# Optimization experiments

Hardware: AMD Instinct MI355X
Metric: run time of the kernel (lower is better)

## Reference

```python
import jax, jax.numpy as jnp
import numpy as np

N_CELL = 66
N_SUB = 29934
N = N_CELL + N_SUB  # 30000 nodes
F = 256
E_HALF = 480000
K = 3
LAYERS = 2
BN_EPS = 1e-5


def setup_inputs() -> dict:
    key = jax.random.key(0)
    ks = jax.random.split(key, 8)
    cell_feat = jax.random.normal(ks[0], (N_CELL, F), dtype=jnp.float32)
    sub_feat = jax.random.normal(ks[1], (N_SUB, F), dtype=jnp.float32)
    # interaction_edge builds a symmetric directed edge list: (a,b) and (b,a)
    src = jax.random.randint(ks[2], (E_HALF,), 0, N)
    dst = jax.random.randint(ks[3], (E_HALF,), 0, N)
    edge_index = jnp.stack([jnp.concatenate([src, dst]),
                            jnp.concatenate([dst, src])], axis=0)
    ew_half = jax.random.uniform(ks[4], (E_HALF,), dtype=jnp.float32, minval=0.1, maxval=1.0)
    edge_weight = jnp.concatenate([ew_half, ew_half])
    glorot = np.sqrt(6.0 / (F + F))
    W1 = jax.random.uniform(ks[5], (F, F), dtype=jnp.float32, minval=-glorot, maxval=glorot)
    W2 = jax.random.uniform(ks[6], (F, F), dtype=jnp.float32, minval=-glorot, maxval=glorot)
    b1 = jnp.zeros((F,), jnp.float32)
    b2 = jnp.zeros((F,), jnp.float32)
    prelu_w = jnp.full((F,), 0.25, jnp.float32)  # PReLU default init
    gamma = jnp.ones((F,), jnp.float32)
    beta = jnp.zeros((F,), jnp.float32)
    return {"cell_feat": cell_feat, "sub_feat": sub_feat,
            "edge_index": edge_index, "edge_weight": edge_weight,
            "W1": W1, "b1": b1, "W2": W2, "b2": b2,
            "prelu_w": prelu_w, "gamma": gamma, "beta": beta}


def _gcn_norm(edge_index, edge_weight, n):
    # SGConv's gcn_norm: add self-loops (weight 1), symmetric degree normalization
    loop = jnp.arange(n)
    row = jnp.concatenate([edge_index[0], loop])  # source j
    col = jnp.concatenate([edge_index[1], loop])  # target i
    ew = jnp.concatenate([edge_weight, jnp.ones((n,), edge_weight.dtype)])
    deg = jax.ops.segment_sum(ew, col, num_segments=n)
    dinv = jnp.where(deg > 0, jax.lax.rsqrt(deg), 0.0)
    norm = dinv[row] * ew * dinv[col]
    return row, col, norm


def _sgconv(x, row, col, norm, W, b, n):
    # K-hop propagation: x <- A_hat^K x, then linear
    for _ in range(K):
        x = jax.ops.segment_sum(norm[:, None] * x[row], col, num_segments=n)
    return x @ W.T + b


def _prelu_bn(x, prelu_w, gamma, beta):
    x = jnp.where(x >= 0, x, prelu_w * x)
    mean = jnp.mean(x, axis=0)
    var = jnp.mean(jnp.square(x - mean), axis=0)  # biased, training-mode BN
    return gamma * (x - mean) * jax.lax.rsqrt(var + BN_EPS) + beta


def reference(cell_feat, sub_feat, edge_index, edge_weight,
              W1, b1, W2, b2, prelu_w, gamma, beta):
    x = jnp.concatenate([cell_feat, sub_feat], axis=0)  # [N, F]
    n = x.shape[0]
    row, col, norm = _gcn_norm(edge_index, edge_weight, n)
    for W, b in ((W1, b1), (W2, b2)):
        x = _sgconv(x, row, col, norm, W, b, n)
        x = _prelu_bn(x, prelu_w, gamma, beta)
    return x[:N_CELL, :], x[N_CELL:, :]
```

## Files before the change

kernel.cpp:

```cpp
#include <hip/hip_runtime.h>
#include <hip/hip_bf16.h>

constexpr int NN    = 30000;
constexpr int NCELL = 66;
constexpr int NF    = 256;
constexpr int CAP   = 80;
constexpr float EPS = 1e-5f;

using bf16x8 = __attribute__((ext_vector_type(8))) short;
using f32x4  = __attribute__((ext_vector_type(4))) float;
using f32x2  = __attribute__((ext_vector_type(2))) float;

__device__ __forceinline__ unsigned short f2bf(float f) {
    __hip_bfloat16 h = __float2bfloat16(f);
    return *reinterpret_cast<unsigned short*>(&h);
}
__device__ __forceinline__ void acc8v(f32x2* acc, float4 u, float w) {
    unsigned a = __float_as_uint(u.x), b = __float_as_uint(u.y);
    unsigned c = __float_as_uint(u.z), d = __float_as_uint(u.w);
    f32x2 wv; wv[0] = w; wv[1] = w;
    f32x2 e0; e0[0] = __uint_as_float(a << 16); e0[1] = __uint_as_float(a & 0xffff0000u);
    f32x2 e1; e1[0] = __uint_as_float(b << 16); e1[1] = __uint_as_float(b & 0xffff0000u);
    f32x2 e2; e2[0] = __uint_as_float(c << 16); e2[1] = __uint_as_float(c & 0xffff0000u);
    f32x2 e3; e3[0] = __uint_as_float(d << 16); e3[1] = __uint_as_float(d & 0xffff0000u);
    acc[0] += wv * e0;
    acc[1] += wv * e1;
    acc[2] += wv * e2;
    acc[3] += wv * e3;
}
__device__ __forceinline__ void acc8(float* acc, float4 u, float w) {
    unsigned a = __float_as_uint(u.x), b = __float_as_uint(u.y);
    unsigned c = __float_as_uint(u.z), d = __float_as_uint(u.w);
    acc[0] += w * __uint_as_float(a << 16);
    acc[1] += w * __uint_as_float(a & 0xffff0000u);
    acc[2] += w * __uint_as_float(b << 16);
    acc[3] += w * __uint_as_float(b & 0xffff0000u);
    acc[4] += w * __uint_as_float(c << 16);
    acc[5] += w * __uint_as_float(c & 0xffff0000u);
    acc[6] += w * __uint_as_float(d << 16);
    acc[7] += w * __uint_as_float(d & 0xffff0000u);
}
__device__ __forceinline__ void edge_meta(const unsigned* p, int& r, float& w) {
    unsigned v = *p;
    r = (int)(v & 0xffffu);
    w = (float)(v >> 16) * (1.0f / 65536.0f);
}
__device__ __forceinline__ void bn_ss(const float* sums, const float* gamma,
                                      const float* beta, int col, float& sc, float& sh) {
    float mean = sums[col] * (1.0f / (float)NN);
    float var  = sums[NF + col] * (1.0f / (float)NN) - mean * mean;
    if (var < 0.f) var = 0.f;
    float istd = rsqrtf(var + EPS);
    sc = gamma[col] * istd;
    sh = beta[col] - mean * sc;
}

__global__ void k_setup(int* fill, float* sums,
                        const float4* __restrict__ W1, ushort4* __restrict__ W1h,
                        const float4* __restrict__ W2, ushort4* __restrict__ W2h) {
    int b = blockIdx.x;
    if (b < 118) {
        int i = b * 256 + threadIdx.x;
        if (i < NN) fill[i] = 0;
        if (i < 2 * NF) sums[i] = 0.0f;
    } else {
        const float4* src = (b < 182) ? W1 : W2;
        ushort4* dst      = (b < 182) ? W1h : W2h;
        int idx = (b - ((b < 182) ? 118 : 182)) * 256 + threadIdx.x;
        if (idx < NF * NF / 4) {
            float4 v = src[idx];
            ushort4 o;
            o.x = f2bf(v.x); o.y = f2bf(v.y); o.z = f2bf(v.z); o.w = f2bf(v.w);
            dst[idx] = o;
        }
    }
}

__global__ void k_zero_stats(float* sums) {
    int i = threadIdx.x;
    if (i < 2 * NF) sums[i] = 0.0f;
}

constexpr int SLICE = 2048;
__global__ __launch_bounds__(256) void k_scatter8(const int* __restrict__ ei,
                                                  const float* __restrict__ ew,
                                                  int* fill, unsigned* __restrict__ bkt,
                                                  int E) {
    int r  = blockIdx.x & 7;
    int s  = blockIdx.x >> 3;
    int lo = r * (NN / 8);
    int hi = lo + (NN / 8);
    int e0 = s * SLICE;
    int e1 = e0 + SLICE; if (e1 > E) e1 = E;
    for (int e = e0 + threadIdx.x; e < e1; e += 256) {
        int col = ei[E + e];
        if (col >= lo && col < hi) {
            int row  = ei[e];
            float wv = ew[e];
            unsigned q = (unsigned)(wv * 65536.0f);
            int pos = atomicAdd(&fill[col], 1);
            bkt[(size_t)col * CAP + pos] = ((unsigned)row) | (q << 16);
        }
    }
}

__global__ void k_deg(const unsigned* __restrict__ bkt, const int* __restrict__ fill,
                      float* __restrict__ s1, float* __restrict__ s2) {
    int i = blockIdx.x * 256 + threadIdx.x;
    if (i >= NN) return;
    int cnt = fill[i];
    unsigned sq = 0;
    const unsigned* p = bkt + (size_t)i * CAP;
    for (int e = 0; e < cnt; e++) sq += (p[e] >> 16);
    float deg = 1.0f + (float)sq * (1.0f / 65536.0f);
    float di = rsqrtf(deg);
    s2[i] = di;
    s1[i] = di * di;
}

__global__ void k_concat_h(const float4* __restrict__ cell, const float4* __restrict__ sub,
                           const float* __restrict__ dinv, ushort4* __restrict__ xh) {
    int idx = blockIdx.x * 256 + threadIdx.x;
    if (idx >= NN * (NF / 4)) return;
    const int CELL4 = NCELL * (NF / 4);
    float4 v = (idx < CELL4) ? cell[idx] : sub[idx - CELL4];
    float di = dinv[idx >> 6];
    ushort4 o;
    o.x = f2bf(v.x * di); o.y = f2bf(v.y * di);
    o.z = f2bf(v.z * di); o.w = f2bf(v.w * di);
    xh[idx] = o;
}

__global__ __launch_bounds__(256) void k_prop(const ushort* __restrict__ xin,
                                              ushort* __restrict__ xout,
                                              const int* __restrict__ fill,
                                              const unsigned* __restrict__ bkt,
                                              const float* __restrict__ scale) {
    int n = blockIdx.x * 4 + (threadIdx.x >> 6);
    int lane = threadIdx.x & 63;
    int half = lane >> 5;
    int fb = lane & 31;
    const float4* xrow = (const float4*)xin;
    const unsigned* base = bkt + (size_t)n * CAP;
    int cnt = fill[n];
    float4 uself = xrow[n * 32 + fb];
    float sc = scale[n];
    f32x2 acc[4];
    #pragma unroll
    for (int i = 0; i < 4; i++) { acc[i][0] = 0.f; acc[i][1] = 0.f; }
    int steps = cnt >> 1;
    int it = 0;
    int e = half;
    if (8 <= steps) {
        unsigned m[8];
        #pragma unroll
        for (int j = 0; j < 8; j++) m[j] = base[e + 2 * j];
        for (;;) {
            int   r[8];
            float w[8];
            #pragma unroll
            for (int j = 0; j < 8; j++) {
                r[j] = (int)(m[j] & 0xffffu);
                w[j] = (float)(m[j] >> 16) * (1.0f / 65536.0f);
            }
            float4 u[8];
            #pragma unroll
            for (int j = 0; j < 8; j++) u[j] = xrow[r[j] * 32 + fb];
            it += 8; e += 16;
            bool more = (it + 8 <= steps);
            if (more) {
                #pragma unroll
                for (int j = 0; j < 8; j++) m[j] = base[e + 2 * j];
            }
            #pragma unroll
            for (int j = 0; j < 8; j++) acc8v(acc, u[j], w[j]);
            if (!more) break;
        }
    }
    for (; it + 4 <= steps; it += 4, e += 8) {
        int r0, r1, r2, r3; float w0, w1, w2, w3;
        edge_meta(base + e,     r0, w0);
        edge_meta(base + e + 2, r1, w1);
        edge_meta(base + e + 4, r2, w2);
        edge_meta(base + e + 6, r3, w3);
        float4 u0 = xrow[r0 * 32 + fb];
        float4 u1 = xrow[r1 * 32 + fb];
        float4 u2 = xrow[r2 * 32 + fb];
        float4 u3 = xrow[r3 * 32 + fb];
        acc8v(acc, u0, w0); acc8v(acc, u1, w1); acc8v(acc, u2, w2); acc8v(acc, u3, w3);
    }
    for (; it < steps; ++it, e += 2) {
        int r0; float w0;
        edge_meta(base + e, r0, w0);
        float4 u0 = xrow[r0 * 32 + fb];
        acc8v(acc, u0, w0);
    }
    if ((cnt & 1) && half == 0) {
        int r0; float w0;
        edge_meta(base + cnt - 1, r0, w0);
        float4 u0 = xrow[r0 * 32 + fb];
        acc8v(acc, u0, w0);
    }
    float accs[8];
    #pragma unroll
    for (int i = 0; i < 4; i++) { accs[2 * i] = acc[i][0]; accs[2 * i + 1] = acc[i][1]; }
    #pragma unroll
    for (int i = 0; i < 8; i++) accs[i] += __shfl_xor(accs[i], 32);
    if (half == 0) {
        acc8(accs, uself, 1.0f);
        #pragma unroll
        for (int i = 0; i < 8; i++) accs[i] *= sc;
        unsigned p0 = ((unsigned)f2bf(accs[1]) << 16) | f2bf(accs[0]);
        unsigned p1 = ((unsigned)f2bf(accs[3]) << 16) | f2bf(accs[2]);
        unsigned p2 = ((unsigned)f2bf(accs[5]) << 16) | f2bf(accs[4]);
        unsigned p3 = ((unsigned)f2bf(accs[7]) << 16) | f2bf(accs[6]);
        float4 o;
        o.x = __uint_as_float(p0); o.y = __uint_as_float(p1);
        o.z = __uint_as_float(p2); o.w = __uint_as_float(p3);
        ((float4*)xout)[n * 32 + fb] = o;
    }
}

__global__ __launch_bounds__(256) void k_gemm_fused(const short* __restrict__ A,
                                                    const short* __restrict__ B,
                                                    const float* __restrict__ bias,
                                                    const float* __restrict__ pw,
                                                    float* __restrict__ y,
                                                    float* __restrict__ sums) {
    constexpr int RT = NN / 16;
    int w    = threadIdx.x >> 6;
    int lane = threadIdx.x & 63;
    int rt   = blockIdx.x * 4 + w;
    int ml   = lane & 15;
    int q    = lane >> 4;
    bool valid = rt < RT;
    __shared__ float red[2][4][NF];
    f32x4 acc[16];
    #pragma unroll
    for (int i = 0; i < 16; i++) acc[i] = (f32x4){0.f, 0.f, 0.f, 0.f};
    if (valid) {
        const short* arow = A + (rt * 16 + ml) * NF + q * 8;
        #pragma unroll
        for (int ks = 0; ks < 8; ks++) {
            bf16x8 a = *(const bf16x8*)(arow + ks * 32);
            #pragma unroll
            for (int nt = 0; nt < 16; nt++) {
                bf16x8 b = *(const bf16x8*)(B + (nt * 16 + ml) * NF + ks * 32 + q * 8);
                acc[nt] = __builtin_amdgcn_mfma_f32_16x16x32_bf16(a, b, acc[nt], 0, 0, 0);
            }
        }
    }
    #pragma unroll
    for (int nt = 0; nt < 16; nt++) {
        int col = nt * 16 + ml;
        float s = 0.f, s2 = 0.f;
        if (valid) {
            float bb = bias[col];
            float pc = pw[col];
            #pragma unroll
            for (int r = 0; r < 4; r++) {
                float v = acc[nt][r] + bb;
                v = (v >= 0.f) ? v : pc * v;
                s += v; s2 += v * v;
                y[(rt * 16 + q * 4 + r) * NF + col] = v;
            }
        }
        s  += __shfl_xor(s, 16);  s  += __shfl_xor(s, 32);
        s2 += __shfl_xor(s2, 16); s2 += __shfl_xor(s2, 32);
        if (lane < 16) { red[0][w][col] = s; red[1][w][col] = s2; }
    }
    __syncthreads();
    int t = threadIdx.x;
    float v0 = red[0][0][t] + red[0][1][t] + red[0][2][t] + red[0][3][t];
    float v1 = red[1][0][t] + red[1][1][t] + red[1][2][t] + red[1][3][t];
    atomicAdd(&sums[t], v0);
    atomicAdd(&sums[NF + t], v1);
}

__global__ void k_apply_h(const float4* __restrict__ y, const float* __restrict__ sums,
                          const float* __restrict__ gamma, const float* __restrict__ beta,
                          const float* __restrict__ dinv, ushort4* __restrict__ xh) {
    int idx = blockIdx.x * 256 + threadIdx.x;
    if (idx >= NN * (NF / 4)) return;
    int f = (idx & 63) * 4;
    float sc0, sh0, sc1, sh1, sc2, sh2, sc3, sh3;
    bn_ss(sums, gamma, beta, f,     sc0, sh0);
    bn_ss(sums, gamma, beta, f + 1, sc1, sh1);
    bn_ss(sums, gamma, beta, f + 2, sc2, sh2);
    bn_ss(sums, gamma, beta, f + 3, sc3, sh3);
    float di = dinv[idx >> 6];
    float4 v = y[idx];
    ushort4 o;
    o.x = f2bf((v.x * sc0 + sh0) * di);
    o.y = f2bf((v.y * sc1 + sh1) * di);
    o.z = f2bf((v.z * sc2 + sh2) * di);
    o.w = f2bf((v.w * sc3 + sh3) * di);
    xh[idx] = o;
}

__global__ void k_apply_out(const float4* __restrict__ y, const float* __restrict__ sums,
                            const float* __restrict__ gamma, const float* __restrict__ beta,
                            float4* __restrict__ out) {
    int idx = blockIdx.x * 256 + threadIdx.x;
    if (idx >= NN * (NF / 4)) return;
    int f = (idx & 63) * 4;
    float sc0, sh0, sc1, sh1, sc2, sh2, sc3, sh3;
    bn_ss(sums, gamma, beta, f,     sc0, sh0);
    bn_ss(sums, gamma, beta, f + 1, sc1, sh1);
    bn_ss(sums, gamma, beta, f + 2, sc2, sh2);
    bn_ss(sums, gamma, beta, f + 3, sc3, sh3);
    float4 v = y[idx];
    float4 o;
    o.x = v.x * sc0 + sh0;
    o.y = v.y * sc1 + sh1;
    o.z = v.z * sc2 + sh2;
    o.w = v.w * sc3 + sh3;
    out[idx] = o;
}

extern "C" void kernel_launch(void* const* d_in, const int* in_sizes, int n_in,
                              void* d_out, int out_size, void* d_ws, size_t ws_size,
                              hipStream_t stream) {
    const float* cell  = (const float*)d_in[0];
    const float* sub   = (const float*)d_in[1];
    const int*   ei    = (const int*)  d_in[2];
    const float* ew    = (const float*)d_in[3];
    const float* W1    = (const float*)d_in[4];
    const float* bias1 = (const float*)d_in[5];
    const float* W2    = (const float*)d_in[6];
    const float* bias2 = (const float*)d_in[7];
    const float* pw    = (const float*)d_in[8];
    const float* gamma = (const float*)d_in[9];
    const float* beta  = (const float*)d_in[10];
    float* out = (float*)d_out;
    const int E = in_sizes[3];

    char* ws = (char*)d_ws;
    size_t off = 0;
    auto alloc = [&](size_t bytes) -> void* {
        void* p = ws + off;
        off = (off + bytes + 255) & ~((size_t)255);
        return p;
    };
    ushort*   xh0  = (ushort*)  alloc((size_t)NN * NF * 2);
    ushort*   xh1  = (ushort*)  alloc((size_t)NN * NF * 2);
    float*    yf   = (float*)   alloc((size_t)NN * NF * 4);
    ushort*   W1h  = (ushort*)  alloc((size_t)NF * NF * 2);
    ushort*   W2h  = (ushort*)  alloc((size_t)NF * NF * 2);
    unsigned* bkt  = (unsigned*)alloc((size_t)NN * CAP * 4);
    int*      fill = (int*)     alloc((size_t)NN * 4);
    float*    s1   = (float*)   alloc((size_t)NN * 4);
    float*    s2   = (float*)   alloc((size_t)NN * 4);
    float*    sums = (float*)   alloc((size_t)2 * NF * 4);

    const int gN  = (NN + 255) / 256;
    const int gSU = 118 + 64 + 64;
    const int gS8 = ((E + SLICE - 1) / SLICE) * 8;
    const int gV4 = (NN * NF / 4 + 255) / 256;
    const int gP  = NN / 4;
    const int gG  = (NN / 16 + 3) / 4;

    k_setup<<<gSU, 256, 0, stream>>>(fill, sums, (const float4*)W1, (ushort4*)W1h,
                                     (const float4*)W2, (ushort4*)W2h);
    k_scatter8<<<gS8, 256, 0, stream>>>(ei, ew, fill, bkt, E);
    k_deg<<<gN, 256, 0, stream>>>(bkt, fill, s1, s2);
    k_concat_h<<<gV4, 256, 0, stream>>>((const float4*)cell, (const float4*)sub, s2, (ushort4*)xh0);

    k_prop<<<gP, 256, 0, stream>>>(xh0, xh1, fill, bkt, s1);
    k_prop<<<gP, 256, 0, stream>>>(xh1, xh0, fill, bkt, s1);
    k_prop<<<gP, 256, 0, stream>>>(xh0, xh1, fill, bkt, s2);
    k_gemm_fused<<<gG, 256, 0, stream>>>((const short*)xh1, (const short*)W1h, bias1, pw, yf, sums);
    k_apply_h<<<gV4, 256, 0, stream>>>((const float4*)yf, sums, gamma, beta, s2, (ushort4*)xh0);
    k_zero_stats<<<1, 512, 0, stream>>>(sums);

    k_prop<<<gP, 256, 0, stream>>>(xh0, xh1, fill, bkt, s1);
    k_prop<<<gP, 256, 0, stream>>>(xh1, xh0, fill, bkt, s1);
    k_prop<<<gP, 256, 0, stream>>>(xh0, xh1, fill, bkt, s2);
    k_gemm_fused<<<gG, 256, 0, stream>>>((const short*)xh1, (const short*)W2h, bias2, pw, yf, sums);
    k_apply_out<<<gV4, 256, 0, stream>>>((const float4*)yf, sums, gamma, beta, (float4*)out);
}
```

Baseline: 624.2 us.

## Fuse degree and concat kernels, store GEMM output as bf16, nontemporal edge loads

Merges the degree computation and the feature concat/scale into one kernel. The old per-node serial sum over the bucket becomes a 32-lane parallel sum with shuffle reduction. The fused GEMM now writes its pre-BN activations in bf16 instead of fp32, which halves the traffic for that buffer in the write and in both apply kernels. Edge metadata loads in the propagation kernel use nontemporal loads to reduce cache pollution. The bf16 intermediate adds rounding error before batch norm, and the BN statistics are still taken from the unrounded values.

```diff
diff --git a/kernel.cpp b/kernel.cpp
--- a/kernel.cpp
+++ b/kernel.cpp
@@ -14,6 +14,9 @@
 __device__ __forceinline__ unsigned short f2bf(float f) {
     __hip_bfloat16 h = __float2bfloat16(f);
     return *reinterpret_cast<unsigned short*>(&h);
+}
+__device__ __forceinline__ float bf2f(unsigned short u) {
+    return __uint_as_float(((unsigned)u) << 16);
 }
 __device__ __forceinline__ void acc8v(f32x2* acc, float4 u, float w) {
     unsigned a = __float_as_uint(u.x), b = __float_as_uint(u.y);
@@ -39,11 +42,6 @@
     acc[5] += w * __uint_as_float(c & 0xffff0000u);
     acc[6] += w * __uint_as_float(d << 16);
     acc[7] += w * __uint_as_float(d & 0xffff0000u);
-}
-__device__ __forceinline__ void edge_meta(const unsigned* p, int& r, float& w) {
-    unsigned v = *p;
-    r = (int)(v & 0xffffu);
-    w = (float)(v >> 16) * (1.0f / 65536.0f);
 }
 __device__ __forceinline__ void bn_ss(const float* sums, const float* gamma,
                                       const float* beta, int col, float& sc, float& sh) {
@@ -104,31 +102,38 @@
     }
 }
 
-__global__ void k_deg(const unsigned* __restrict__ bkt, const int* __restrict__ fill,
-                      float* __restrict__ s1, float* __restrict__ s2) {
-    int i = blockIdx.x * 256 + threadIdx.x;
-    if (i >= NN) return;
-    int cnt = fill[i];
+__global__ __launch_bounds__(256) void k_degcat(const unsigned* __restrict__ bkt,
+                                                const int* __restrict__ fill,
+                                                const float4* __restrict__ cell,
+                                                const float4* __restrict__ sub,
+                                                float* __restrict__ s1,
+                                                float* __restrict__ s2,
+                                                ushort4* __restrict__ xh) {
+    int g  = threadIdx.x >> 5;
+    int l  = threadIdx.x & 31;
+    int n  = blockIdx.x * 8 + g;
+    int cnt = fill[n];
+    const unsigned* p = bkt + (size_t)n * CAP;
     unsigned sq = 0;
-    const unsigned* p = bkt + (size_t)i * CAP;
-    for (int e = 0; e < cnt; e++) sq += (p[e] >> 16);
+    for (int e = l; e < cnt; e += 32) sq += (p[e] >> 16);
+    sq += __shfl_xor((int)sq, 1);
+    sq += __shfl_xor((int)sq, 2);
+    sq += __shfl_xor((int)sq, 4);
+    sq += __shfl_xor((int)sq, 8);
+    sq += __shfl_xor((int)sq, 16);
     float deg = 1.0f + (float)sq * (1.0f / 65536.0f);
     float di = rsqrtf(deg);
-    s2[i] = di;
-    s1[i] = di * di;
-}
-
-__global__ void k_concat_h(const float4* __restrict__ cell, const float4* __restrict__ sub,
-                           const float* __restrict__ dinv, ushort4* __restrict__ xh) {
-    int idx = blockIdx.x * 256 + threadIdx.x;
-    if (idx >= NN * (NF / 4)) return;
+    if (l == 0) { s2[n] = di; s1[n] = di * di; }
     const int CELL4 = NCELL * (NF / 4);
-    float4 v = (idx < CELL4) ? cell[idx] : sub[idx - CELL4];
-    float di = dinv[idx >> 6];
-    ushort4 o;
-    o.x = f2bf(v.x * di); o.y = f2bf(v.y * di);
-    o.z = f2bf(v.z * di); o.w = f2bf(v.w * di);
-    xh[idx] = o;
+    #pragma unroll
+    for (int k = 0; k < 2; k++) {
+        int gidx = n * 64 + l + 32 * k;
+        float4 v = (gidx < CELL4) ? cell[gidx] : sub[gidx - CELL4];
+        ushort4 o;
+        o.x = f2bf(v.x * di); o.y = f2bf(v.y * di);
+        o.z = f2bf(v.z * di); o.w = f2bf(v.w * di);
+        xh[gidx] = o;
+    }
 }
 
 __global__ __launch_bounds__(256) void k_prop(const ushort* __restrict__ xin,
@@ -154,7 +159,7 @@
     if (8 <= steps) {
         unsigned m[8];
         #pragma unroll
-        for (int j = 0; j < 8; j++) m[j] = base[e + 2 * j];
+        for (int j = 0; j < 8; j++) m[j] = __builtin_nontemporal_load(base + e + 2 * j);
         for (;;) {
             int   r[8];
             float w[8];
@@ -170,7 +175,7 @@
             bool more = (it + 8 <= steps);
             if (more) {
                 #pragma unroll
-                for (int j = 0; j < 8; j++) m[j] = base[e + 2 * j];
+                for (int j = 0; j < 8; j++) m[j] = __builtin_nontemporal_load(base + e + 2 * j);
             }
             #pragma unroll
             for (int j = 0; j < 8; j++) acc8v(acc, u[j], w[j]);
@@ -178,11 +183,16 @@
         }
     }
     for (; it + 4 <= steps; it += 4, e += 8) {
-        int r0, r1, r2, r3; float w0, w1, w2, w3;
-        edge_meta(base + e,     r0, w0);
-        edge_meta(base + e + 2, r1, w1);
-        edge_meta(base + e + 4, r2, w2);
-        edge_meta(base + e + 6, r3, w3);
+        unsigned m0 = __builtin_nontemporal_load(base + e);
+        unsigned m1 = __builtin_nontemporal_load(base + e + 2);
+        unsigned m2 = __builtin_nontemporal_load(base + e + 4);
+        unsigned m3 = __builtin_nontemporal_load(base + e + 6);
+        int r0 = (int)(m0 & 0xffffu), r1 = (int)(m1 & 0xffffu);
+        int r2 = (int)(m2 & 0xffffu), r3 = (int)(m3 & 0xffffu);
+        float w0 = (float)(m0 >> 16) * (1.0f / 65536.0f);
+        float w1 = (float)(m1 >> 16) * (1.0f / 65536.0f);
+        float w2 = (float)(m2 >> 16) * (1.0f / 65536.0f);
+        float w3 = (float)(m3 >> 16) * (1.0f / 65536.0f);
         float4 u0 = xrow[r0 * 32 + fb];
         float4 u1 = xrow[r1 * 32 + fb];
         float4 u2 = xrow[r2 * 32 + fb];
@@ -190,14 +200,16 @@
         acc8v(acc, u0, w0); acc8v(acc, u1, w1); acc8v(acc, u2, w2); acc8v(acc, u3, w3);
     }
     for (; it < steps; ++it, e += 2) {
-        int r0; float w0;
-        edge_meta(base + e, r0, w0);
+        unsigned m0 = __builtin_nontemporal_load(base + e);
+        int r0 = (int)(m0 & 0xffffu);
+        float w0 = (float)(m0 >> 16) * (1.0f / 65536.0f);
         float4 u0 = xrow[r0 * 32 + fb];
         acc8v(acc, u0, w0);
     }
     if ((cnt & 1) && half == 0) {
-        int r0; float w0;
-        edge_meta(base + cnt - 1, r0, w0);
+        unsigned m0 = __builtin_nontemporal_load(base + cnt - 1);
+        int r0 = (int)(m0 & 0xffffu);
+        float w0 = (float)(m0 >> 16) * (1.0f / 65536.0f);
         float4 u0 = xrow[r0 * 32 + fb];
         acc8v(acc, u0, w0);
     }
@@ -225,7 +237,7 @@
                                                     const short* __restrict__ B,
                                                     const float* __restrict__ bias,
                                                     const float* __restrict__ pw,
-                                                    float* __restrict__ y,
+                                                    ushort* __restrict__ yh,
                                                     float* __restrict__ sums) {
     constexpr int RT = NN / 16;
     int w    = threadIdx.x >> 6;
@@ -262,7 +274,7 @@
                 float v = acc[nt][r] + bb;
                 v = (v >= 0.f) ? v : pc * v;
                 s += v; s2 += v * v;
-                y[(rt * 16 + q * 4 + r) * NF + col] = v;
+                yh[(rt * 16 + q * 4 + r) * NF + col] = f2bf(v);
             }
         }
         s  += __shfl_xor(s, 16);  s  += __shfl_xor(s, 32);
@@ -277,7 +289,7 @@
     atomicAdd(&sums[NF + t], v1);
 }
 
-__global__ void k_apply_h(const float4* __restrict__ y, const float* __restrict__ sums,
+__global__ void k_apply_h(const ushort4* __restrict__ yh, const float* __restrict__ sums,
                           const float* __restrict__ gamma, const float* __restrict__ beta,
                           const float* __restrict__ dinv, ushort4* __restrict__ xh) {
     int idx = blockIdx.x * 256 + threadIdx.x;
@@ -289,16 +301,16 @@
     bn_ss(sums, gamma, beta, f + 2, sc2, sh2);
     bn_ss(sums, gamma, beta, f + 3, sc3, sh3);
     float di = dinv[idx >> 6];
-    float4 v = y[idx];
+    ushort4 v = yh[idx];
     ushort4 o;
-    o.x = f2bf((v.x * sc0 + sh0) * di);
-    o.y = f2bf((v.y * sc1 + sh1) * di);
-    o.z = f2bf((v.z * sc2 + sh2) * di);
-    o.w = f2bf((v.w * sc3 + sh3) * di);
+    o.x = f2bf((bf2f(v.x) * sc0 + sh0) * di);
+    o.y = f2bf((bf2f(v.y) * sc1 + sh1) * di);
+    o.z = f2bf((bf2f(v.z) * sc2 + sh2) * di);
+    o.w = f2bf((bf2f(v.w) * sc3 + sh3) * di);
     xh[idx] = o;
 }
 
-__global__ void k_apply_out(const float4* __restrict__ y, const float* __restrict__ sums,
+__global__ void k_apply_out(const ushort4* __restrict__ yh, const float* __restrict__ sums,
                             const float* __restrict__ gamma, const float* __restrict__ beta,
                             float4* __restrict__ out) {
     int idx = blockIdx.x * 256 + threadIdx.x;
@@ -309,12 +321,12 @@
     bn_ss(sums, gamma, beta, f + 1, sc1, sh1);
     bn_ss(sums, gamma, beta, f + 2, sc2, sh2);
     bn_ss(sums, gamma, beta, f + 3, sc3, sh3);
-    float4 v = y[idx];
+    ushort4 v = yh[idx];
     float4 o;
-    o.x = v.x * sc0 + sh0;
-    o.y = v.y * sc1 + sh1;
-    o.z = v.z * sc2 + sh2;
-    o.w = v.w * sc3 + sh3;
+    o.x = bf2f(v.x) * sc0 + sh0;
+    o.y = bf2f(v.y) * sc1 + sh1;
+    o.z = bf2f(v.z) * sc2 + sh2;
+    o.w = bf2f(v.w) * sc3 + sh3;
     out[idx] = o;
 }
 
@@ -344,7 +356,7 @@
     };
     ushort*   xh0  = (ushort*)  alloc((size_t)NN * NF * 2);
     ushort*   xh1  = (ushort*)  alloc((size_t)NN * NF * 2);
-    float*    yf   = (float*)   alloc((size_t)NN * NF * 4);
+    ushort*   yh   = (ushort*)  alloc((size_t)NN * NF * 2);
     ushort*   W1h  = (ushort*)  alloc((size_t)NF * NF * 2);
     ushort*   W2h  = (ushort*)  alloc((size_t)NF * NF * 2);
     unsigned* bkt  = (unsigned*)alloc((size_t)NN * CAP * 4);
@@ -353,9 +365,9 @@
     float*    s2   = (float*)   alloc((size_t)NN * 4);
     float*    sums = (float*)   alloc((size_t)2 * NF * 4);
 
-    const int gN  = (NN + 255) / 256;
     const int gSU = 118 + 64 + 64;
     const int gS8 = ((E + SLICE - 1) / SLICE) * 8;
+    const int gDC = NN / 8;
     const int gV4 = (NN * NF / 4 + 255) / 256;
     const int gP  = NN / 4;
     const int gG  = (NN / 16 + 3) / 4;
@@ -363,19 +375,19 @@
     k_setup<<<gSU, 256, 0, stream>>>(fill, sums, (const float4*)W1, (ushort4*)W1h,
                                      (const float4*)W2, (ushort4*)W2h);
     k_scatter8<<<gS8, 256, 0, stream>>>(ei, ew, fill, bkt, E);
-    k_deg<<<gN, 256, 0, stream>>>(bkt, fill, s1, s2);
-    k_concat_h<<<gV4, 256, 0, stream>>>((const float4*)cell, (const float4*)sub, s2, (ushort4*)xh0);
+    k_degcat<<<gDC, 256, 0, stream>>>(bkt, fill, (const float4*)cell, (const float4*)sub,
+                                      s1, s2, (ushort4*)xh0);
 
     k_prop<<<gP, 256, 0, stream>>>(xh0, xh1, fill, bkt, s1);
     k_prop<<<gP, 256, 0, stream>>>(xh1, xh0, fill, bkt, s1);
     k_prop<<<gP, 256, 0, stream>>>(xh0, xh1, fill, bkt, s2);
-    k_gemm_fused<<<gG, 256, 0, stream>>>((const short*)xh1, (const short*)W1h, bias1, pw, yf, sums);
-    k_apply_h<<<gV4, 256, 0, stream>>>((const float4*)yf, sums, gamma, beta, s2, (ushort4*)xh0);
+    k_gemm_fused<<<gG, 256, 0, stream>>>((const short*)xh1, (const short*)W1h, bias1, pw, yh, sums);
+    k_apply_h<<<gV4, 256, 0, stream>>>((const ushort4*)yh, sums, gamma, beta, s2, (ushort4*)xh0);
     k_zero_stats<<<1, 512, 0, stream>>>(sums);
 
     k_prop<<<gP, 256, 0, stream>>>(xh0, xh1, fill, bkt, s1);
     k_prop<<<gP, 256, 0, stream>>>(xh1, xh0, fill, bkt, s1);
     k_prop<<<gP, 256, 0, stream>>>(xh0, xh1, fill, bkt, s2);
-    k_gemm_fused<<<gG, 256, 0, stream>>>((const short*)xh1, (const short*)W2h, bias2, pw, yf, sums);
-    k_apply_out<<<gV4, 256, 0, stream>>>((const float4*)yf, sums, gamma, beta, (float4*)out);
-}
+    k_gemm_fused<<<gG, 256, 0, stream>>>((const short*)xh1, (const short*)W2h, bias2, pw, yh, sums);
+    k_apply_out<<<gV4, 256, 0, stream>>>((const ushort4*)yh, sums, gamma, beta, (float4*)out);
+}
```

Result: no change. 621.4 us (-0.4%).
